# Performance work log

Measured on AMD Instinct MI355X. Metric: run time of the kernel, lower is better.

Reference implementation:

```python
import jax, jax.numpy as jnp
import numpy as np

EPS = 1e-5  # torch LayerNorm default
H = 8       # heads_num


def _ln(t, g, b):
    m = jnp.mean(t, axis=-1, keepdims=True)
    v = jnp.var(t, axis=-1, keepdims=True)
    return (t - m) / jnp.sqrt(v + EPS) * g + b


def setup_inputs() -> dict:
    key = jax.random.key(0)
    ks = jax.random.split(key, 12)
    B, S, Dq, Dk, Dff = 4, 2048, 512, 768, 2048
    def w(k, shape, scale=0.02):
        return jax.random.normal(k, shape, jnp.float32) * scale
    return {
        "x": jax.random.normal(ks[0], (B, S, Dq), jnp.float32),
        "y": jax.random.normal(ks[1], (B, S, Dk), jnp.float32),
        # cross-attention projections (stored [in, out]; linear_q/k/v have no bias)
        "Wq": w(ks[2], (Dq, Dq)), "Wk": w(ks[3], (Dk, Dq)), "Wv": w(ks[4], (Dk, Dq)),
        "Wo": w(ks[5], (Dq, Dq)), "bo": jnp.zeros((Dq,), jnp.float32),
        # nn.MultiheadAttention packed in-projection and out-projection
        "mha_w_in": w(ks[6], (Dq, 3 * Dq)), "mha_b_in": jnp.zeros((3 * Dq,), jnp.float32),
        "mha_wo": w(ks[7], (Dq, Dq)), "mha_bo": jnp.zeros((Dq,), jnp.float32),
        # 4 LayerNorms
        "ln1_g": jnp.ones((Dq,), jnp.float32), "ln1_b": jnp.zeros((Dq,), jnp.float32),
        "ln2_g": jnp.ones((Dk,), jnp.float32), "ln2_b": jnp.zeros((Dk,), jnp.float32),
        "ln3_g": jnp.ones((Dq,), jnp.float32), "ln3_b": jnp.zeros((Dq,), jnp.float32),
        "ln4_g": jnp.ones((Dq,), jnp.float32), "ln4_b": jnp.zeros((Dq,), jnp.float32),
        # dense MLP (moe=False branch)
        "mlp_w1": w(ks[8], (Dq, Dff)), "mlp_b1": jnp.zeros((Dff,), jnp.float32),
        "mlp_w2": w(ks[9], (Dff, Dq)), "mlp_b2": jnp.zeros((Dq,), jnp.float32),
    }


def reference(x, y, Wq, Wk, Wv, Wo, bo, mha_w_in, mha_b_in, mha_wo, mha_bo,
              ln1_g, ln1_b, ln2_g, ln2_b, ln3_g, ln3_b, ln4_g, ln4_b,
              mlp_w1, mlp_b1, mlp_w2, mlp_b2):
    B, S, D = x.shape
    hd = D // H
    inv_sqrt_hd = 1.0 / np.sqrt(hd).astype(np.float32)

    xn = _ln(x, ln1_g, ln1_b)
    yn = _ln(y, ln2_g, ln2_b)

    # ---- Multi_CrossAttention: manual QK^T softmax V over true seq axis ----
    q = (xn @ Wq).reshape(B, S, H, hd)
    k = (yn @ Wk).reshape(B, -1, H, hd)
    v = (yn @ Wv).reshape(B, -1, H, hd)
    scores = jnp.einsum('bqhd,bkhd->bhqk', q, k) * inv_sqrt_hd  # [B,H,S,S] (512 MB)
    attn = jax.nn.softmax(scores, axis=-1)
    ctx = jnp.einsum('bhqk,bkhd->bqhd', attn, v).reshape(B, S, D)
    ca = ctx @ Wo + bo

    h = _ln(ca + xn, ln3_g, ln3_b)

    # ---- nn.MultiheadAttention (batch_first=False!): axis 0 is the sequence ----
    qkv = h @ mha_w_in + mha_b_in  # [L=B, N=S, 3D]
    q2, k2, v2 = jnp.split(qkv, 3, axis=-1)
    L, N = q2.shape[0], q2.shape[1]
    q2 = q2.reshape(L, N, H, hd)
    k2 = k2.reshape(L, N, H, hd)
    v2 = v2.reshape(L, N, H, hd)
    s2 = jnp.einsum('lnhd,mnhd->nhlm', q2, k2) * inv_sqrt_hd  # [N,H,L,L]
    a2 = jax.nn.softmax(s2, axis=-1)
    sa = jnp.einsum('nhlm,mnhd->lnhd', a2, v2).reshape(L, N, D) @ mha_wo + mha_bo

    h2 = _ln(sa + h, ln4_g, ln4_b)

    # ---- dense MLP (GELU exact, dropout=0) ----
    mlp = jax.nn.gelu(h2 @ mlp_w1 + mlp_b1, approximate=False) @ mlp_w2 + mlp_b2
    return mlp + h2
```

## Files before the change

### kernel.cpp

```cpp
#include <hip/hip_runtime.h>
#include <math.h>

typedef unsigned short u16;
typedef __attribute__((ext_vector_type(8))) short bf8;
typedef __attribute__((ext_vector_type(4))) float f4;
typedef __attribute__((ext_vector_type(4))) unsigned int u32x4;
typedef __attribute__((ext_vector_type(2))) unsigned int u32x2;
typedef __attribute__((ext_vector_type(4))) unsigned short u16x4;
typedef __attribute__((ext_vector_type(8))) unsigned short u16x8;

__device__ __forceinline__ float bf2f(u16 a){
  unsigned u = ((unsigned)a) << 16;
  float f; __builtin_memcpy(&f, &u, 4);
  return f;
}
__device__ __forceinline__ u16 f2bf(float f){
  unsigned u; __builtin_memcpy(&u, &f, 4);
  u += 0x7fffu + ((u >> 16) & 1u);
  return (u16)(u >> 16);
}
__device__ __forceinline__ unsigned packbf(float a, float b){
  unsigned ua, ub;
  __builtin_memcpy(&ua, &a, 4); __builtin_memcpy(&ub, &b, 4);
  ua += 0x8000u; ub += 0x8000u;
  return __builtin_amdgcn_perm(ub, ua, 0x07060302u);
}
__device__ __forceinline__ void gload16(const u16* g, u16* l){
  __builtin_amdgcn_global_load_lds((const __attribute__((address_space(1))) void*)g,
                                   (__attribute__((address_space(3))) void*)l, 16, 0, 0);
}
__device__ __forceinline__ int xcd_swizzle(int orig, int nwg){
  const int qq = nwg >> 3, rr = nwg & 7;
  const int xcd = orig & 7, loc = orig >> 3;
  return (xcd < rr ? xcd * (qq + 1) : rr * (qq + 1) + (xcd - rr) * qq) + loc;
}

__global__ void k_transpose_all(
    const float* __restrict__ Wq, const float* __restrict__ Wk,
    const float* __restrict__ Wv, const float* __restrict__ Wo,
    const float* __restrict__ Win, const float* __restrict__ Wmo,
    const float* __restrict__ W1, const float* __restrict__ W2,
    u16* __restrict__ WqT, u16* __restrict__ WkT, u16* __restrict__ WvT,
    u16* __restrict__ WoT, u16* __restrict__ WinT, u16* __restrict__ WmoT,
    u16* __restrict__ W1T, u16* __restrict__ W2T)
{
  __shared__ float tile[32][33];
  const int tid = blockIdx.x;
  const float* in; u16* out; int R, C, lo;
  if (tid < 1280){
    if (tid < 256)       { in = Wq;  out = WqT;  R = 512; C = 512;  lo = 0; }
    else if (tid < 640)  { in = Wk;  out = WkT;  R = 768; C = 512;  lo = 256; }
    else if (tid < 1024) { in = Wv;  out = WvT;  R = 768; C = 512;  lo = 640; }
    else                 { in = Wo;  out = WoT;  R = 512; C = 512;  lo = 1024; }
  } else {
    if (tid < 2048)      { in = Win; out = WinT; R = 512; C = 1536; lo = 1280; }
    else if (tid < 2304) { in = Wmo; out = WmoT; R = 512; C = 512;  lo = 2048; }
    else if (tid < 3328) { in = W1;  out = W1T;  R = 512; C = 2048; lo = 2304; }
    else                 { in = W2;  out = W2T;  R = 2048; C = 512; lo = 3328; }
  }
  const int local = tid - lo;
  const int tpx = C >> 5;
  const int bx = (local % tpx) * 32, by = (local / tpx) * 32;
  const int tx = threadIdx.x, ty = threadIdx.y;
#pragma unroll
  for (int i = 0; i < 4; i++)
    tile[ty + i*8][tx] = in[(size_t)(by + ty + i*8) * C + bx + tx];
  __syncthreads();
#pragma unroll
  for (int i = 0; i < 4; i++)
    out[(size_t)(bx + ty + i*8) * R + by + tx] = f2bf(tile[tx][ty + i*8]);
}

__device__ __forceinline__ void ln_row(
    const float* __restrict__ r, const float* __restrict__ gam,
    const float* __restrict__ bet, float* __restrict__ outf,
    u16* __restrict__ outb, int D, int t)
{
  const int nv = D >> 8;
  float v[3] = {0.f, 0.f, 0.f};
  float s = 0.f, s2 = 0.f;
#pragma unroll
  for (int i = 0; i < 3; i++){
    if (i < nv){ float xx = r[t + i*256]; v[i] = xx; s += xx; s2 += xx*xx; }
  }
#pragma unroll
  for (int m = 32; m; m >>= 1){ s += __shfl_xor(s, m); s2 += __shfl_xor(s2, m); }
  __shared__ float rs[4], rq[4];
  const int wave = t >> 6;
  if ((t & 63) == 0){ rs[wave] = s; rq[wave] = s2; }
  __syncthreads();
  s  = rs[0] + rs[1] + rs[2] + rs[3];
  s2 = rq[0] + rq[1] + rq[2] + rq[3];
  const float mean = s / (float)D;
  const float var  = s2 / (float)D - mean * mean;
  const float rstd = rsqrtf(var + 1e-5f);
#pragma unroll
  for (int i = 0; i < 3; i++){
    if (i < nv){
      const int c = t + i*256;
      float o = (v[i] - mean) * rstd * gam[c] + bet[c];
      if (outf) outf[c] = o;
      outb[c] = f2bf(o);
    }
  }
}

__global__ __launch_bounds__(256) void k_layernorm(
    const float* __restrict__ in, const float* __restrict__ gam,
    const float* __restrict__ bet, float* __restrict__ outf,
    u16* __restrict__ outb, int D)
{
  const int row = blockIdx.x;
  ln_row(in + (size_t)row * D, gam, bet,
         outf ? outf + (size_t)row * D : nullptr,
         outb + (size_t)row * D, D, threadIdx.x);
}

__global__ __launch_bounds__(256) void k_layernorm12(
    const float* __restrict__ x, const float* __restrict__ y,
    const float* __restrict__ g1, const float* __restrict__ b1,
    const float* __restrict__ g2, const float* __restrict__ b2,
    float* __restrict__ xnF, u16* __restrict__ xnB, u16* __restrict__ ynB)
{
  const int row = blockIdx.x;
  if (row < 8192){
    ln_row(x + (size_t)row * 512, g1, b1, xnF + (size_t)row * 512,
           xnB + (size_t)row * 512, 512, threadIdx.x);
  } else {
    const int r2 = row - 8192;
    ln_row(y + (size_t)r2 * 768, g2, b2, nullptr,
           ynB + (size_t)r2 * 768, 768, threadIdx.x);
  }
}

template<int TM, int TN, bool BIAS, bool RES, bool GELU_ACT, int OUTM>
__global__ __launch_bounds__(256, 4) void k_gemm(
    const u16* __restrict__ A, const u16* __restrict__ BT,
    const float* __restrict__ bias, const float* __restrict__ res,
    float* __restrict__ outf, u16* __restrict__ outb, u16* __restrict__ outb2,
    int M, int N, int K)
{
  constexpr int MF = TM / 32;
  constexpr int NF = TN / 32;
  constexpr int WM = TM / 2;
  constexpr int WN = TN / 2;
  __shared__ u16 Sb[(TM + TN) * 64];
  const int t = threadIdx.x;
  const int gx = gridDim.x;
  const int swz = xcd_swizzle(blockIdx.y * gx + blockIdx.x, gx * gridDim.y);
  const int m0 = (swz / gx) * TM, n0 = (swz % gx) * TN;
  const int wave = t >> 6, lane = t & 63;
  const int wm = wave >> 1, wn = wave & 1;
  const int l15 = lane & 15, lg = lane >> 4;
  const u16* Ag = A + (size_t)m0 * K;
  const u16* Bg = BT + (size_t)n0 * K;

  const int lrow = lane >> 3;
  const int csrc = (((lane & 7) ^ lrow) << 3);
  const u16* Agl = Ag + (size_t)lrow * K + csrc;
  const u16* Bgl = Bg + (size_t)lrow * K + csrc;

  f4 acc[MF][NF];
#pragma unroll
  for (int i = 0; i < MF; i++)
#pragma unroll
    for (int j = 0; j < NF; j++) acc[i][j] = (f4){0.f, 0.f, 0.f, 0.f};

  const int nK = K >> 6;
#pragma unroll
  for (int i = 0; i < TM/32; i++){
    const int rb = (i*4 + wave) * 8;
    gload16(Agl + (size_t)rb * K, &Sb[rb * 64]);
  }
#pragma unroll
  for (int i = 0; i < TN/32; i++){
    const int rb = (i*4 + wave) * 8;
    gload16(Bgl + (size_t)rb * K, &Sb[(TM + rb) * 64]);
  }
  asm volatile("s_waitcnt vmcnt(0)" ::: "memory");
  __syncthreads();

  for (int kt = 0;; kt++){
    const char* As = (const char*)&Sb[0];
    const char* Bs = (const char*)&Sb[TM * 64];
#pragma unroll
    for (int kc = 0; kc < 2; kc++){
      bf8 af[MF], bfr[NF];
      const int kb = kc*64 + lg*16;
#pragma unroll
      for (int mf = 0; mf < MF; mf++){
        const int row = wm*WM + mf*16 + l15;
        af[mf] = *(const bf8*)(As + row*128 + (kb ^ ((row & 7) << 4)));
      }
#pragma unroll
      for (int nf = 0; nf < NF; nf++){
        const int row = wn*WN + nf*16 + l15;
        bfr[nf] = *(const bf8*)(Bs + row*128 + (kb ^ ((row & 7) << 4)));
      }
#pragma unroll
      for (int mf = 0; mf < MF; mf++)
#pragma unroll
        for (int nf = 0; nf < NF; nf++)
          acc[mf][nf] = __builtin_amdgcn_mfma_f32_16x16x32_bf16(af[mf], bfr[nf], acc[mf][nf], 0, 0, 0);
    }
    if (kt + 1 == nK) break;
    __syncthreads();
    const int ko = (kt + 1) << 6;
#pragma unroll
    for (int i = 0; i < TM/32; i++){
      const int rb = (i*4 + wave) * 8;
      gload16(Agl + (size_t)rb * K + ko, &Sb[rb * 64]);
    }
#pragma unroll
    for (int i = 0; i < TN/32; i++){
      const int rb = (i*4 + wave) * 8;
      gload16(Bgl + (size_t)rb * K + ko, &Sb[(TM + rb) * 64]);
    }
    asm volatile("s_waitcnt vmcnt(0)" ::: "memory");
    __syncthreads();
  }
#pragma unroll
  for (int mf = 0; mf < MF; mf++){
#pragma unroll
    for (int nf = 0; nf < NF; nf++){
      const int colg = n0 + wn*WN + nf*16 + l15;
      const int rowg = m0 + wm*WM + mf*16 + lg*4;
      const float bv = BIAS ? bias[colg] : 0.f;
      float vv[4];
#pragma unroll
      for (int j = 0; j < 4; j++){
        float v = acc[mf][nf][j] + bv;
        if (RES) v += res[(size_t)(rowg + j) * N + colg];
        if (GELU_ACT) v = 0.5f * v * (1.f + erff(v * 0.7071067811865475f));
        vv[j] = v;
      }
      if (OUTM == 0){
#pragma unroll
        for (int j = 0; j < 4; j++) outf[(size_t)(rowg + j) * N + colg] = vv[j];
      } else if (OUTM == 1){
#pragma unroll
        for (int j = 0; j < 4; j++) outb[(size_t)(rowg + j) * N + colg] = f2bf(vv[j]);
      } else if (OUTM == 2){
        const int bb = rowg >> 11, ss = rowg & 2047;
        u16x4 pk;
#pragma unroll
        for (int j = 0; j < 4; j++) pk[j] = f2bf(vv[j]);
        *(u16x4*)(outb + ((size_t)(bb*512 + colg)) * 2048 + ss) = pk;
      } else {
        if (n0 < 512){
#pragma unroll
          for (int j = 0; j < 4; j++) outb[(size_t)(rowg + j) * 512 + colg] = f2bf(vv[j]);
        } else {
          const int bb = rowg >> 11, ss = rowg & 2047;
          u16x4 pk;
#pragma unroll
          for (int j = 0; j < 4; j++) pk[j] = f2bf(vv[j]);
          *(u16x4*)(outb2 + ((size_t)(bb*512 + (colg - 512))) * 2048 + ss) = pk;
        }
      }
    }
  }
}

__global__ __launch_bounds__(256, 4) void k_flash(
    const u16* __restrict__ q, const u16* __restrict__ k,
    const u16* __restrict__ vt, u16* __restrict__ ctx)
{
  __shared__ u16 Kb[2][64 * 64];
  __shared__ u16 Vb[2][64 * 64];
  __shared__ char Pb[4][16 * 128];
  const int t = threadIdx.x;
  const int wave = t >> 6, lane = t & 63;
  const int l15 = lane & 15, lg = lane >> 4;
  const int id = blockIdx.y * 32 + blockIdx.x;
  const int swz = xcd_swizzle(id, 1024);
  const int qb = swz & 31, bh = swz >> 5;
  const int b = bh >> 3, h = bh & 7;
  const int qrow0 = qb*64 + wave*16;
  constexpr float CEXP = 0.125f * 1.44269504f;

  const u16* qp = q + ((size_t)(b*2048 + qrow0 + l15)) * 512 + h*64 + lg*8;
  const bf8 qf0 = *(const bf8*)qp;
  const bf8 qf1 = *(const bf8*)(qp + 32);

  const int lrow = lane >> 3;
  const int csrc = (((lane & 7) ^ lrow) << 3);
  const u16* kgl = k  + ((size_t)(b*2048 + lrow)) * 512  + h*64 + csrc;
  const u16* vgl = vt + ((size_t)(b*512 + h*64 + lrow)) * 2048 + csrc;

#pragma unroll
  for (int i = 0; i < 2; i++){
    const int rb = (i*4 + wave) * 8;
    gload16(kgl + (size_t)rb * 512,  &Kb[0][rb * 64]);
    gload16(vgl + (size_t)rb * 2048, &Vb[0][rb * 64]);
  }

  f4 o[4];
#pragma unroll
  for (int nb = 0; nb < 4; nb++) o[nb] = (f4){0.f,0.f,0.f,0.f};
  float rl = 0.f;
  char* myp = Pb[wave];
  const int psw = (l15 & 7) << 4;

  int cur = 0;
  for (int it = 0; it < 32; it++){
    asm volatile("s_waitcnt vmcnt(0)" ::: "memory");
    __syncthreads();
    if (it + 1 < 32){
      const int kt = (it + 1) << 6;
#pragma unroll
      for (int i = 0; i < 2; i++){
        const int rb = (i*4 + wave) * 8;
        gload16(kgl + (size_t)(kt + rb) * 512,  &Kb[cur^1][rb * 64]);
        gload16(vgl + (size_t)rb * 2048 + kt,   &Vb[cur^1][rb * 64]);
      }
    }
    const char* kbuf = (const char*)Kb[cur];
    const char* vbuf = (const char*)Vb[cur];
    f4 s[4];
    __builtin_amdgcn_s_setprio(1);
#pragma unroll
    for (int nb = 0; nb < 4; nb++){
      const int row = nb*16 + l15;
      const int sx = (row & 7) << 4;
      const bf8 kf0 = *(const bf8*)(kbuf + row*128 + ((lg*16) ^ sx));
      const bf8 kf1 = *(const bf8*)(kbuf + row*128 + ((64 + lg*16) ^ sx));
      f4 a = (f4){0.f,0.f,0.f,0.f};
      a = __builtin_amdgcn_mfma_f32_16x16x32_bf16(kf0, qf0, a, 0, 0, 0);
      a = __builtin_amdgcn_mfma_f32_16x16x32_bf16(kf1, qf1, a, 0, 0, 0);
      s[nb] = a;
    }
    __builtin_amdgcn_s_setprio(0);
    float p[4][4];
#pragma unroll
    for (int nb = 0; nb < 4; nb++)
#pragma unroll
      for (int j = 0; j < 4; j++)
        p[nb][j] = __builtin_amdgcn_exp2f(s[nb][j] * CEXP);
    float ts = ((p[0][0]+p[1][0]) + (p[2][0]+p[3][0]))
             + ((p[0][1]+p[1][1]) + (p[2][1]+p[3][1]))
             + ((p[0][2]+p[1][2]) + (p[2][2]+p[3][2]))
             + ((p[0][3]+p[1][3]) + (p[2][3]+p[3][3]));
    ts += __shfl_xor(ts, 16);
    ts += __shfl_xor(ts, 32);
    rl += ts;
#pragma unroll
    for (int nb = 0; nb < 4; nb++){
      u32x2 w;
      w[0] = packbf(p[nb][0], p[nb][1]);
      w[1] = packbf(p[nb][2], p[nb][3]);
      *(u32x2*)(myp + l15*128 + ((nb*32 + lg*8) ^ psw)) = w;
    }
    asm volatile("s_waitcnt lgkmcnt(0)" ::: "memory");
    __builtin_amdgcn_sched_barrier(0);
    const bf8 pf0 = *(const bf8*)(myp + l15*128 + ((lg*16) ^ psw));
    const bf8 pf1 = *(const bf8*)(myp + l15*128 + ((64 + lg*16) ^ psw));
    bf8 vf[4][2];
#pragma unroll
    for (int nb = 0; nb < 4; nb++){
      const int row = nb*16 + l15;
      const int sx = (row & 7) << 4;
      vf[nb][0] = *(const bf8*)(vbuf + row*128 + ((lg*16) ^ sx));
      vf[nb][1] = *(const bf8*)(vbuf + row*128 + ((64 + lg*16) ^ sx));
    }
    __builtin_amdgcn_s_setprio(1);
#pragma unroll
    for (int nb = 0; nb < 4; nb++){
      o[nb] = __builtin_amdgcn_mfma_f32_16x16x32_bf16(pf0, vf[nb][0], o[nb], 0, 0, 0);
      o[nb] = __builtin_amdgcn_mfma_f32_16x16x32_bf16(pf1, vf[nb][1], o[nb], 0, 0, 0);
    }
    __builtin_amdgcn_s_setprio(0);
    cur ^= 1;
  }
  const float i0 = 1.f / __shfl(rl, lg*4 + 0);
  const float i1 = 1.f / __shfl(rl, lg*4 + 1);
  const float i2 = 1.f / __shfl(rl, lg*4 + 2);
  const float i3 = 1.f / __shfl(rl, lg*4 + 3);
#pragma unroll
  for (int nb = 0; nb < 4; nb++){
    u16* cp = ctx + ((size_t)(b*2048 + qrow0 + lg*4)) * 512 + h*64 + nb*16 + l15;
    cp[0]    = f2bf(o[nb][0] * i0);
    cp[512]  = f2bf(o[nb][1] * i1);
    cp[1024] = f2bf(o[nb][2] * i2);
    cp[1536] = f2bf(o[nb][3] * i3);
  }
}

__global__ __launch_bounds__(256) void k_mha_small(const u16* __restrict__ qkv,
                                                   u16* __restrict__ outb)
{
  const int tid = blockIdx.x * 256 + threadIdx.x;
  const int n = tid & 2047;
  const int hl = tid >> 11;
  const int h = hl >> 2, l = hl & 3;
  const u16* qp = qkv + ((size_t)l * 2048 + n) * 1536 + h*64;
  float qv[64];
#pragma unroll
  for (int i = 0; i < 8; i++){
    const bf8 c = *(const bf8*)(qp + i*8);
#pragma unroll
    for (int j2 = 0; j2 < 8; j2++) qv[i*8 + j2] = bf2f((u16)c[j2]) * 0.125f;
  }
  float sc[4];
#pragma unroll
  for (int m = 0; m < 4; m++){
    const u16* kp = qkv + ((size_t)m * 2048 + n) * 1536 + 512 + h*64;
    float a = 0.f;
#pragma unroll
    for (int i = 0; i < 8; i++){
      const bf8 c = *(const bf8*)(kp + i*8);
#pragma unroll
      for (int j2 = 0; j2 < 8; j2++) a += qv[i*8 + j2] * bf2f((u16)c[j2]);
    }
    sc[m] = a;
  }
  const float mx = fmaxf(fmaxf(sc[0], sc[1]), fmaxf(sc[2], sc[3]));
  float p[4]; float sum = 0.f;
#pragma unroll
  for (int m = 0; m < 4; m++){ p[m] = __expf(sc[m] - mx); sum += p[m]; }
  const float inv = 1.f / sum;
  float ov[64];
#pragma unroll
  for (int i = 0; i < 64; i++) ov[i] = 0.f;
#pragma unroll
  for (int m = 0; m < 4; m++){
    const float pw = p[m] * inv;
    const u16* vp = qkv + ((size_t)m * 2048 + n) * 1536 + 1024 + h*64;
#pragma unroll
    for (int i = 0; i < 8; i++){
      const bf8 c = *(const bf8*)(vp + i*8);
#pragma unroll
      for (int j2 = 0; j2 < 8; j2++) ov[i*8 + j2] += pw * bf2f((u16)c[j2]);
    }
  }
  u16* op = outb + ((size_t)l * 2048 + n) * 512 + h*64;
#pragma unroll
  for (int i = 0; i < 8; i++){
    u16x8 pk;
#pragma unroll
    for (int j2 = 0; j2 < 8; j2++) pk[j2] = f2bf(ov[i*8 + j2]);
    *(u16x8*)(op + i*8) = pk;
  }
}

extern "C" void kernel_launch(void* const* d_in, const int* in_sizes, int n_in,
                              void* d_out, int out_size, void* d_ws, size_t ws_size,
                              hipStream_t stream)
{
  (void)in_sizes; (void)n_in; (void)out_size; (void)ws_size;
  const float* x    = (const float*)d_in[0];
  const float* y    = (const float*)d_in[1];
  const float* Wq   = (const float*)d_in[2];
  const float* Wk   = (const float*)d_in[3];
  const float* Wv   = (const float*)d_in[4];
  const float* Wo   = (const float*)d_in[5];
  const float* bo   = (const float*)d_in[6];
  const float* Win  = (const float*)d_in[7];
  const float* bin  = (const float*)d_in[8];
  const float* Wmo  = (const float*)d_in[9];
  const float* bmo  = (const float*)d_in[10];
  const float* ln1g = (const float*)d_in[11];
  const float* ln1b = (const float*)d_in[12];
  const float* ln2g = (const float*)d_in[13];
  const float* ln2b = (const float*)d_in[14];
  const float* ln3g = (const float*)d_in[15];
  const float* ln3b = (const float*)d_in[16];
  const float* ln4g = (const float*)d_in[17];
  const float* ln4b = (const float*)d_in[18];
  const float* W1   = (const float*)d_in[19];
  const float* b1   = (const float*)d_in[20];
  const float* W2   = (const float*)d_in[21];
  const float* b2   = (const float*)d_in[22];

  char* ws = (char*)d_ws;
  const size_t MB = 1024 * 1024;
  u16* WqT  = (u16*)ws;
  u16* WkT  = WqT  + 512 * 512;
  u16* WvT  = WkT  + 512 * 768;
  u16* WoT  = WvT  + 512 * 768;
  u16* WinT = WoT  + 512 * 512;
  u16* WmoT = WinT + 1536 * 512;
  u16* W1T  = WmoT + 512 * 512;
  u16* W2T  = W1T  + 2048 * 512;
  float* hF   = (float*)(ws + 9 * MB);
  float* xnF  = (float*)(ws + 25 * MB);
  float* carF = (float*)(ws + 41 * MB);
  u16* xnB  = (u16*)(ws + 57 * MB);
  u16* ynB  = (u16*)(ws + 65 * MB);
  u16* qB   = (u16*)(ws + 77 * MB);
  u16* kB   = (u16*)(ws + 85 * MB);
  u16* vtB  = (u16*)(ws + 93 * MB);
  u16* ctxB = (u16*)(ws + 101 * MB);
  float* sarF = xnF;
  float* h2F  = carF;
  u16* saB   = xnB;
  u16* hB    = ynB;
  u16* h2B   = qB;
  u16* qkvB  = kB;
  u16* t1B   = (u16*)hF;

  k_transpose_all<<<4352, dim3(32, 8), 0, stream>>>(
      Wq, Wk, Wv, Wo, Win, Wmo, W1, W2,
      WqT, WkT, WvT, WoT, WinT, WmoT, W1T, W2T);

  k_layernorm12<<<16384, 256, 0, stream>>>(x, y, ln1g, ln1b, ln2g, ln2b,
                                           xnF, xnB, ynB);

  k_gemm<64,128,false,false,false,1><<<dim3(4, 128), 256, 0, stream>>>(xnB, WqT, nullptr, nullptr, nullptr, qB, nullptr, 8192, 512, 512);
  k_gemm<64,128,false,false,false,3><<<dim3(8, 128), 256, 0, stream>>>(ynB, WkT, nullptr, nullptr, nullptr, kB, vtB,   8192, 1024, 768);

  k_flash<<<dim3(32, 32), 256, 0, stream>>>(qB, kB, vtB, ctxB);

  k_gemm<64,128,true,true,false,0><<<dim3(4, 128), 256, 0, stream>>>(ctxB, WoT, bo, xnF, carF, nullptr, nullptr, 8192, 512, 512);
  k_layernorm<<<8192, 256, 0, stream>>>(carF, ln3g, ln3b, hF, hB, 512);

  k_gemm<128,128,true,false,false,1><<<dim3(12, 64), 256, 0, stream>>>(hB, WinT, bin, nullptr, nullptr, qkvB, nullptr, 8192, 1536, 512);
  k_mha_small<<<256, 256, 0, stream>>>(qkvB, saB);
  k_gemm<64,128,true,true,false,0><<<dim3(4, 128), 256, 0, stream>>>(saB, WmoT, bmo, hF, sarF, nullptr, nullptr, 8192, 512, 512);
  k_layernorm<<<8192, 256, 0, stream>>>(sarF, ln4g, ln4b, h2F, h2B, 512);

  k_gemm<128,128,true,false,true,1><<<dim3(16, 64), 256, 0, stream>>>(h2B, W1T, b1, nullptr, nullptr, t1B, nullptr, 8192, 2048, 512);
  k_gemm<64,128,true,true,false,0><<<dim3(4, 128), 256, 0, stream>>>(t1B, W2T, b2, h2F, (float*)d_out, nullptr, nullptr, 8192, 512, 2048);
}
```

Baseline: 242.1 us.

## Rework flash attention onto 32x32 MFMA with in-register P via permlane swap

The flash kernel now uses 32x32x16 bf16 MFMA tiles with 128 query rows per block. The QK^T result layout is converted into the A-operand layout for the PV product with v_cvt_pk_bf16_f32 and v_permlane32_swap, so the per-wave LDS round-trip for P goes away. The softmax scale times log2(e) is folded into the Q projection epilogue, which removes the per-element multiply in the flash loop. In exchange, register pressure rises (launch bounds drop to 2 blocks per CU), the grid halves, and the kernel depends on gfx950-specific instructions.

```diff
diff --git a/kernel.cpp b/kernel.cpp
--- a/kernel.cpp
+++ b/kernel.cpp
@@ -4,6 +4,7 @@
 typedef unsigned short u16;
 typedef __attribute__((ext_vector_type(8))) short bf8;
 typedef __attribute__((ext_vector_type(4))) float f4;
+typedef __attribute__((ext_vector_type(16))) float f32x16;
 typedef __attribute__((ext_vector_type(4))) unsigned int u32x4;
 typedef __attribute__((ext_vector_type(2))) unsigned int u32x2;
 typedef __attribute__((ext_vector_type(4))) unsigned short u16x4;
@@ -19,11 +20,13 @@
   u += 0x7fffu + ((u >> 16) & 1u);
   return (u16)(u >> 16);
 }
-__device__ __forceinline__ unsigned packbf(float a, float b){
-  unsigned ua, ub;
-  __builtin_memcpy(&ua, &a, 4); __builtin_memcpy(&ub, &b, 4);
-  ua += 0x8000u; ub += 0x8000u;
-  return __builtin_amdgcn_perm(ub, ua, 0x07060302u);
+__device__ __forceinline__ unsigned cvtpk(float a, float b){
+  unsigned r;
+  asm("v_cvt_pk_bf16_f32 %0, %1, %2" : "=v"(r) : "v"(a), "v"(b));
+  return r;
+}
+__device__ __forceinline__ void plswap(unsigned &a, unsigned &b){
+  asm("v_permlane32_swap_b32 %0, %1" : "+v"(a), "+v"(b));
 }
 __device__ __forceinline__ void gload16(const u16* g, u16* l){
   __builtin_amdgcn_global_load_lds((const __attribute__((address_space(1))) void*)g,
@@ -133,7 +136,7 @@
   }
 }
 
-template<int TM, int TN, bool BIAS, bool RES, bool GELU_ACT, int OUTM>
+template<int TM, int TN, bool BIAS, bool RES, bool GELU_ACT, int OUTM, bool QSC = false>
 __global__ __launch_bounds__(256, 4) void k_gemm(
     const u16* __restrict__ A, const u16* __restrict__ BT,
     const float* __restrict__ bias, const float* __restrict__ res,
@@ -232,6 +235,7 @@
         float v = acc[mf][nf][j] + bv;
         if (RES) v += res[(size_t)(rowg + j) * N + colg];
         if (GELU_ACT) v = 0.5f * v * (1.f + erff(v * 0.7071067811865475f));
+        if (QSC) v *= 0.1803368801f;
         vv[j] = v;
       }
       if (OUTM == 0){
@@ -262,26 +266,29 @@
   }
 }
 
-__global__ __launch_bounds__(256, 4) void k_flash(
+__global__ __launch_bounds__(256, 2) void k_flash(
     const u16* __restrict__ q, const u16* __restrict__ k,
     const u16* __restrict__ vt, u16* __restrict__ ctx)
 {
   __shared__ u16 Kb[2][64 * 64];
   __shared__ u16 Vb[2][64 * 64];
-  __shared__ char Pb[4][16 * 128];
   const int t = threadIdx.x;
   const int wave = t >> 6, lane = t & 63;
-  const int l15 = lane & 15, lg = lane >> 4;
-  const int id = blockIdx.y * 32 + blockIdx.x;
-  const int swz = xcd_swizzle(id, 1024);
-  const int qb = swz & 31, bh = swz >> 5;
+  const int l31 = lane & 31, hi = lane >> 5;
+  const int id = blockIdx.y * 16 + blockIdx.x;
+  const int swz = xcd_swizzle(id, 512);
+  const int qb = swz & 15, bh = swz >> 4;
   const int b = bh >> 3, h = bh & 7;
-  const int qrow0 = qb*64 + wave*16;
-  constexpr float CEXP = 0.125f * 1.44269504f;
-
-  const u16* qp = q + ((size_t)(b*2048 + qrow0 + l15)) * 512 + h*64 + lg*8;
-  const bf8 qf0 = *(const bf8*)qp;
-  const bf8 qf1 = *(const bf8*)(qp + 32);
+  const int qrow0 = qb*128 + wave*32;
+
+  bf8 qf[4];
+  {
+    const u16* qp = q + ((size_t)(b*2048 + qrow0 + l31)) * 512 + h*64 + hi*8;
+    qf[0] = *(const bf8*)qp;
+    qf[1] = *(const bf8*)(qp + 16);
+    qf[2] = *(const bf8*)(qp + 32);
+    qf[3] = *(const bf8*)(qp + 48);
+  }
 
   const int lrow = lane >> 3;
   const int csrc = (((lane & 7) ^ lrow) << 3);
@@ -295,12 +302,10 @@
     gload16(vgl + (size_t)rb * 2048, &Vb[0][rb * 64]);
   }
 
-  f4 o[4];
-#pragma unroll
-  for (int nb = 0; nb < 4; nb++) o[nb] = (f4){0.f,0.f,0.f,0.f};
+  f32x16 o0, o1;
+#pragma unroll
+  for (int r = 0; r < 16; r++){ o0[r] = 0.f; o1[r] = 0.f; }
   float rl = 0.f;
-  char* myp = Pb[wave];
-  const int psw = (l15 & 7) << 4;
 
   int cur = 0;
   for (int it = 0; it < 32; it++){
@@ -317,72 +322,69 @@
     }
     const char* kbuf = (const char*)Kb[cur];
     const char* vbuf = (const char*)Vb[cur];
-    f4 s[4];
+    f32x16 s0, s1;
+#pragma unroll
+    for (int r = 0; r < 16; r++){ s0[r] = 0.f; s1[r] = 0.f; }
     __builtin_amdgcn_s_setprio(1);
 #pragma unroll
-    for (int nb = 0; nb < 4; nb++){
-      const int row = nb*16 + l15;
-      const int sx = (row & 7) << 4;
-      const bf8 kf0 = *(const bf8*)(kbuf + row*128 + ((lg*16) ^ sx));
-      const bf8 kf1 = *(const bf8*)(kbuf + row*128 + ((64 + lg*16) ^ sx));
-      f4 a = (f4){0.f,0.f,0.f,0.f};
-      a = __builtin_amdgcn_mfma_f32_16x16x32_bf16(kf0, qf0, a, 0, 0, 0);
-      a = __builtin_amdgcn_mfma_f32_16x16x32_bf16(kf1, qf1, a, 0, 0, 0);
-      s[nb] = a;
+    for (int ds = 0; ds < 4; ds++){
+      const int off = ds*32 + hi*16;
+      const int row0 = l31, row1 = 32 + l31;
+      const bf8 kf0 = *(const bf8*)(kbuf + row0*128 + (off ^ ((row0 & 7) << 4)));
+      const bf8 kf1 = *(const bf8*)(kbuf + row1*128 + (off ^ ((row1 & 7) << 4)));
+      s0 = __builtin_amdgcn_mfma_f32_32x32x16_bf16(kf0, qf[ds], s0, 0, 0, 0);
+      s1 = __builtin_amdgcn_mfma_f32_32x32x16_bf16(kf1, qf[ds], s1, 0, 0, 0);
     }
     __builtin_amdgcn_s_setprio(0);
-    float p[4][4];
-#pragma unroll
-    for (int nb = 0; nb < 4; nb++)
-#pragma unroll
-      for (int j = 0; j < 4; j++)
-        p[nb][j] = __builtin_amdgcn_exp2f(s[nb][j] * CEXP);
-    float ts = ((p[0][0]+p[1][0]) + (p[2][0]+p[3][0]))
-             + ((p[0][1]+p[1][1]) + (p[2][1]+p[3][1]))
-             + ((p[0][2]+p[1][2]) + (p[2][2]+p[3][2]))
-             + ((p[0][3]+p[1][3]) + (p[2][3]+p[3][3]));
-    ts += __shfl_xor(ts, 16);
-    ts += __shfl_xor(ts, 32);
-    rl += ts;
-#pragma unroll
-    for (int nb = 0; nb < 4; nb++){
-      u32x2 w;
-      w[0] = packbf(p[nb][0], p[nb][1]);
-      w[1] = packbf(p[nb][2], p[nb][3]);
-      *(u32x2*)(myp + l15*128 + ((nb*32 + lg*8) ^ psw)) = w;
-    }
-    asm volatile("s_waitcnt lgkmcnt(0)" ::: "memory");
-    __builtin_amdgcn_sched_barrier(0);
-    const bf8 pf0 = *(const bf8*)(myp + l15*128 + ((lg*16) ^ psw));
-    const bf8 pf1 = *(const bf8*)(myp + l15*128 + ((64 + lg*16) ^ psw));
-    bf8 vf[4][2];
-#pragma unroll
-    for (int nb = 0; nb < 4; nb++){
-      const int row = nb*16 + l15;
-      const int sx = (row & 7) << 4;
-      vf[nb][0] = *(const bf8*)(vbuf + row*128 + ((lg*16) ^ sx));
-      vf[nb][1] = *(const bf8*)(vbuf + row*128 + ((64 + lg*16) ^ sx));
+    float p0[16], p1[16];
+#pragma unroll
+    for (int r = 0; r < 16; r++){
+      p0[r] = __builtin_amdgcn_exp2f(s0[r]);
+      p1[r] = __builtin_amdgcn_exp2f(s1[r]);
+    }
+    float sum = 0.f;
+#pragma unroll
+    for (int r = 0; r < 16; r++) sum += p0[r] + p1[r];
+    sum += __shfl_xor(sum, 32);
+    rl += sum;
+    bf8 pa[2][2];
+#pragma unroll
+    for (int sub = 0; sub < 2; sub++){
+      const float* pp = sub ? p1 : p0;
+      unsigned w0 = cvtpk(pp[0],  pp[1]),  w1 = cvtpk(pp[2],  pp[3]);
+      unsigned w2 = cvtpk(pp[4],  pp[5]),  w3 = cvtpk(pp[6],  pp[7]);
+      unsigned w4 = cvtpk(pp[8],  pp[9]),  w5 = cvtpk(pp[10], pp[11]);
+      unsigned w6 = cvtpk(pp[12], pp[13]), w7 = cvtpk(pp[14], pp[15]);
+      plswap(w0, w2); plswap(w1, w3);
+      plswap(w4, w6); plswap(w5, w7);
+      u32x4 t0 = {w0, w1, w2, w3};
+      u32x4 t1 = {w4, w5, w6, w7};
+      __builtin_memcpy(&pa[sub][0], &t0, 16);
+      __builtin_memcpy(&pa[sub][1], &t1, 16);
     }
     __builtin_amdgcn_s_setprio(1);
 #pragma unroll
-    for (int nb = 0; nb < 4; nb++){
-      o[nb] = __builtin_amdgcn_mfma_f32_16x16x32_bf16(pf0, vf[nb][0], o[nb], 0, 0, 0);
-      o[nb] = __builtin_amdgcn_mfma_f32_16x16x32_bf16(pf1, vf[nb][1], o[nb], 0, 0, 0);
-    }
+    for (int sub = 0; sub < 2; sub++)
+#pragma unroll
+      for (int kt2 = 0; kt2 < 2; kt2++){
+        const int off = sub*64 + kt2*32 + hi*16;
+        const int row0 = l31, row1 = 32 + l31;
+        const bf8 vf0 = *(const bf8*)(vbuf + row0*128 + (off ^ ((row0 & 7) << 4)));
+        const bf8 vf1 = *(const bf8*)(vbuf + row1*128 + (off ^ ((row1 & 7) << 4)));
+        o0 = __builtin_amdgcn_mfma_f32_32x32x16_bf16(pa[sub][kt2], vf0, o0, 0, 0, 0);
+        o1 = __builtin_amdgcn_mfma_f32_32x32x16_bf16(pa[sub][kt2], vf1, o1, 0, 0, 0);
+      }
     __builtin_amdgcn_s_setprio(0);
     cur ^= 1;
   }
-  const float i0 = 1.f / __shfl(rl, lg*4 + 0);
-  const float i1 = 1.f / __shfl(rl, lg*4 + 1);
-  const float i2 = 1.f / __shfl(rl, lg*4 + 2);
-  const float i3 = 1.f / __shfl(rl, lg*4 + 3);
-#pragma unroll
-  for (int nb = 0; nb < 4; nb++){
-    u16* cp = ctx + ((size_t)(b*2048 + qrow0 + lg*4)) * 512 + h*64 + nb*16 + l15;
-    cp[0]    = f2bf(o[nb][0] * i0);
-    cp[512]  = f2bf(o[nb][1] * i1);
-    cp[1024] = f2bf(o[nb][2] * i2);
-    cp[1536] = f2bf(o[nb][3] * i3);
+  const float linv = 1.f / rl;
+#pragma unroll
+  for (int r = 0; r < 16; r++){
+    const int crow = (r & 3) + 8*(r >> 2) + 4*hi;
+    const float iv = __shfl(linv, crow);
+    u16* cp = ctx + ((size_t)(b*2048 + qrow0 + crow)) * 512 + h*64 + l31;
+    cp[0]  = f2bf(o0[r] * iv);
+    cp[32] = f2bf(o1[r] * iv);
   }
 }
 
@@ -506,10 +508,10 @@
   k_layernorm12<<<16384, 256, 0, stream>>>(x, y, ln1g, ln1b, ln2g, ln2b,
                                            xnF, xnB, ynB);
 
-  k_gemm<64,128,false,false,false,1><<<dim3(4, 128), 256, 0, stream>>>(xnB, WqT, nullptr, nullptr, nullptr, qB, nullptr, 8192, 512, 512);
+  k_gemm<64,128,false,false,false,1,true><<<dim3(4, 128), 256, 0, stream>>>(xnB, WqT, nullptr, nullptr, nullptr, qB, nullptr, 8192, 512, 512);
   k_gemm<64,128,false,false,false,3><<<dim3(8, 128), 256, 0, stream>>>(ynB, WkT, nullptr, nullptr, nullptr, kB, vtB,   8192, 1024, 768);
 
-  k_flash<<<dim3(32, 32), 256, 0, stream>>>(qB, kB, vtB, ctxB);
+  k_flash<<<dim3(16, 32), 256, 0, stream>>>(qB, kB, vtB, ctxB);
 
   k_gemm<64,128,true,true,false,0><<<dim3(4, 128), 256, 0, stream>>>(ctxB, WoT, bo, xnF, carF, nullptr, nullptr, 8192, 512, 512);
   k_layernorm<<<8192, 256, 0, stream>>>(carF, ln3g, ln3b, hF, hB, 512);
```

Result: faster. 232.3 us (-4.0%).
